# Kernel tuning notes

Measured on AMD Instinct MI355X. Metric: run time of the kernel, lower is better.

Reference implementation:

```python
import jax, jax.numpy as jnp
import numpy as np

N_HEAD = 8
D_MODEL = 128  # per-head dim == d_model in this 'interpretable' MHA
B, S = 2, 2048
LN_EPS = 1e-3  # keras LayerNormalization default epsilon


def setup_inputs() -> dict:
    key = jax.random.key(0)
    ks = jax.random.split(key, 8)
    sc = 1.0 / np.sqrt(D_MODEL)
    q = jax.random.normal(ks[0], (B, S, D_MODEL), jnp.float32)
    k = jax.random.normal(ks[1], (B, S, D_MODEL), jnp.float32)
    v = jax.random.normal(ks[2], (B, S, D_MODEL), jnp.float32)
    # multiplicative causal mask (lower-triangular ones), broadcast over B,H
    mask = jnp.tril(jnp.ones((S, S), jnp.float32))[None, None, :, :]
    Wq = jax.random.normal(ks[3], (D_MODEL, N_HEAD * D_MODEL), jnp.float32) * sc
    Wk = jax.random.normal(ks[4], (D_MODEL, N_HEAD * D_MODEL), jnp.float32) * sc
    Wv = jax.random.normal(ks[5], (D_MODEL, N_HEAD * D_MODEL), jnp.float32) * sc
    Wo = jax.random.normal(ks[6], (N_HEAD * D_MODEL, D_MODEL), jnp.float32) * sc
    gamma = jnp.ones((D_MODEL,), jnp.float32)
    beta = jnp.zeros((D_MODEL,), jnp.float32)
    return {"q": q, "k": k, "v": v, "mask": mask, "Wq": Wq, "Wk": Wk,
            "Wv": Wv, "Wo": Wo, "gamma": gamma, "beta": beta}


def reference(q, k, v, mask, Wq, Wk, Wv, Wo, gamma, beta):
    b = q.shape[0]
    # projections -> [B, H, S, D]
    def split_heads(x):
        return x.reshape(b, -1, N_HEAD, D_MODEL).transpose(0, 2, 1, 3)
    qs = split_heads(q @ Wq)
    ks_ = split_heads(k @ Wk)
    vs = split_heads(v @ Wv)
    scores = jnp.einsum('bhqd,bhkd->bhqk', qs, ks_) / jnp.sqrt(jnp.float32(D_MODEL))
    scores = scores * mask  # multiplicative mask (NOT additive -inf)
    attn = jax.nn.softmax(scores, axis=-1)
    # dropout layers are identity at inference
    out = jnp.einsum('bhqk,bhkd->bhqd', attn, vs)
    out = out.transpose(0, 2, 1, 3).reshape(b, -1, N_HEAD * D_MODEL)
    out = out @ Wo
    # keras LayerNorm (axis=-1, eps=1e-3)
    mu = jnp.mean(out, axis=-1, keepdims=True)
    var = jnp.var(out, axis=-1, keepdims=True)
    out = (out - mu) * jax.lax.rsqrt(var + LN_EPS) * gamma + beta
    return out
```

## Files before the change

### kernel.cpp

```cpp
#include <hip/hip_runtime.h>
#include <math.h>

#define B 2
#define S 2048
#define H 8
#define D 128
#define DM 1024
#define BH 16

typedef unsigned short u16;
typedef __attribute__((ext_vector_type(8))) short bf16x8;
typedef __attribute__((ext_vector_type(8))) unsigned short u16x8;
typedef __attribute__((ext_vector_type(4))) float f32x4;

__device__ __forceinline__ float bf2f(u16 x) {
    union { unsigned u; float f; } c; c.u = ((unsigned)x) << 16; return c.f;
}
__device__ __forceinline__ u16 f2bf(float f) {
    union { unsigned u; float f; } c; c.f = f;
    unsigned u = c.u; u += 0x7fffu + ((u >> 16) & 1u);
    return (u16)(u >> 16);
}
__device__ __forceinline__ u16 ftr(float f) {
    union { unsigned u; float f; } c; c.f = f;
    return (u16)(c.u >> 16);
}

#define MFMA16(a, b, c) __builtin_amdgcn_mfma_f32_16x16x32_bf16((a), (b), (c), 0, 0, 0)

__global__ __launch_bounds__(256) void prep_kernel(
    const float* __restrict__ Wq, const float* __restrict__ Wk, const float* __restrict__ Wv,
    const float* __restrict__ Wo, u16* __restrict__ WT, u16* __restrict__ WoT)
{
    __shared__ __align__(16) u16 Wl[128][132];
    int tid = threadIdx.x, by = blockIdx.x;
    if (by < 16) {
        int k0 = by * 64;
#pragma unroll
        for (int i = 0; i < 8; i++) {
            int e = i * 256 + tid; int kk = e >> 5, n4 = e & 31;
            float4 w4 = *(const float4*)&Wo[(size_t)(k0 + kk) * D + n4 * 4];
            ushort4 p; p.x = ftr(w4.x); p.y = ftr(w4.y); p.z = ftr(w4.z); p.w = ftr(w4.w);
            *(ushort4*)&Wl[kk][n4 * 4] = p;
        }
        __syncthreads();
#pragma unroll
        for (int i = 0; i < 4; i++) {
            int e = i * 256 + tid; int n = e >> 3, ko = e & 7;
            u16x8 g;
#pragma unroll
            for (int j = 0; j < 8; j++) g[j] = Wl[ko * 8 + j][n];
            *(u16x8*)&WoT[(size_t)n * DM + k0 + ko * 8] = g;
        }
    } else {
        int tile = by - 16;
        int t = tile >> 3, h = tile & 7;
        const float* W = (t == 0) ? Wq : (t == 1) ? Wk : Wv;
        int col0 = h * 128;
#pragma unroll
        for (int i = 0; i < 16; i++) {
            int e = i * 256 + tid; int kk = e >> 5, n4 = e & 31;
            float4 w4 = *(const float4*)&W[(size_t)kk * DM + col0 + n4 * 4];
            ushort4 p; p.x = ftr(w4.x); p.y = ftr(w4.y); p.z = ftr(w4.z); p.w = ftr(w4.w);
            *(ushort4*)&Wl[kk][n4 * 4] = p;
        }
        __syncthreads();
        u16* WTt = WT + (size_t)tile * (128 * 128);
#pragma unroll
        for (int i = 0; i < 8; i++) {
            int e = i * 256 + tid; int n = e >> 4, ko = e & 15;
            u16x8 g;
#pragma unroll
            for (int j = 0; j < 8; j++) g[j] = Wl[ko * 8 + j][n];
            *(u16x8*)&WTt[(size_t)n * 128 + ko * 8] = g;
        }
    }
}

__global__ __launch_bounds__(256) void proj_kernel(
    const float* __restrict__ q, const float* __restrict__ k, const float* __restrict__ v,
    const u16* __restrict__ WT,
    u16* __restrict__ Qo, u16* __restrict__ Ko, u16* __restrict__ VTo,
    float* __restrict__ Csum)
{
    __shared__ __align__(16) u16 Xs[128][136];
    __shared__ __align__(16) u16 Ws[128][136];
    int tid = threadIdx.x;
    int m0 = blockIdx.x * 128;
    int by = blockIdx.y;
    int t = by >> 3;
    int h = by & 7;
    const float* X = (t == 0) ? q : (t == 1) ? k : v;
    const u16* WTt = WT + (size_t)(t * 8 + h) * (128 * 128);

#pragma unroll
    for (int i = 0; i < 16; i++) {
        int e = i * 256 + tid; int r = e >> 5, c4 = e & 31;
        float4 x4 = *(const float4*)&X[(size_t)(m0 + r) * D + c4 * 4];
        ushort4 p; p.x = ftr(x4.x); p.y = ftr(x4.y); p.z = ftr(x4.z); p.w = ftr(x4.w);
        *(ushort4*)&Xs[r][c4 * 4] = p;
    }
#pragma unroll
    for (int i = 0; i < 8; i++) {
        int e = i * 256 + tid; int n = e >> 4, c8 = e & 15;
        *(u16x8*)&Ws[n][c8 * 8] = *(const u16x8*)&WTt[(size_t)n * 128 + c8 * 8];
    }
    __syncthreads();

    int w = tid >> 6, lane = tid & 63, quad = lane >> 4, ln = lane & 15;
    bf16x8 aX[2][4];
#pragma unroll
    for (int rf = 0; rf < 2; rf++)
#pragma unroll
        for (int ks = 0; ks < 4; ks++)
            aX[rf][ks] = *(const bf16x8*)&Xs[w * 32 + rf * 16 + ln][ks * 32 + quad * 8];

    f32x4 zero = {0.f, 0.f, 0.f, 0.f};
    f32x4 acc[2][8];
#pragma unroll
    for (int rf = 0; rf < 2; rf++)
#pragma unroll
        for (int nt = 0; nt < 8; nt++) acc[rf][nt] = zero;

#pragma unroll
    for (int ks = 0; ks < 4; ks++) {
        bf16x8 bW[8];
#pragma unroll
        for (int nt = 0; nt < 8; nt++)
            bW[nt] = *(const bf16x8*)&Ws[nt * 16 + ln][ks * 32 + quad * 8];
#pragma unroll
        for (int nt = 0; nt < 8; nt++) {
            acc[0][nt] = MFMA16(aX[0][ks], bW[nt], acc[0][nt]);
            acc[1][nt] = MFMA16(aX[1][ks], bW[nt], acc[1][nt]);
        }
    }

    int bb = m0 >> 11, ss0 = m0 & 2047;
    int bh = bb * 8 + h;
    __syncthreads();
    u16 (*Ct)[136] = Xs;
    if (t < 2) {
        u16* O = (t == 0) ? Qo : Ko;
#pragma unroll
        for (int rf = 0; rf < 2; rf++)
#pragma unroll
            for (int nt = 0; nt < 8; nt++)
#pragma unroll
                for (int r = 0; r < 4; r++)
                    Ct[w * 32 + rf * 16 + quad * 4 + r][nt * 16 + ln] = f2bf(acc[rf][nt][r]);
        __syncthreads();
#pragma unroll
        for (int i = 0; i < 8; i++) {
            int e = i * 256 + tid; int r = e >> 4, c8 = e & 15;
            *(u16x8*)&O[((size_t)bh * S + ss0 + r) * D + c8 * 8] = *(const u16x8*)&Ct[r][c8 * 8];
        }
    } else {
#pragma unroll
        for (int rf = 0; rf < 2; rf++)
#pragma unroll
            for (int nt = 0; nt < 8; nt++)
#pragma unroll
                for (int r = 0; r < 4; r++)
                    Ct[nt * 16 + ln][w * 32 + rf * 16 + quad * 4 + r] = f2bf(acc[rf][nt][r]);
        __syncthreads();
#pragma unroll
        for (int i = 0; i < 8; i++) {
            int e = i * 256 + tid; int dloc = e >> 4, s8 = e & 15;
            *(u16x8*)&VTo[((size_t)bh * D + dloc) * S + ss0 + s8 * 8] =
                *(const u16x8*)&Ct[dloc][s8 * 8];
        }
        {
            int d = tid >> 1, c = tid & 1;
            float s = 0.f;
#pragma unroll
            for (int i = 0; i < 8; i++) {
                u16x8 v8 = *(const u16x8*)&Ct[d][c * 64 + i * 8];
#pragma unroll
                for (int j = 0; j < 8; j++) s += bf2f(v8[j]);
            }
            Csum[((size_t)bh * 32 + (ss0 >> 6) + c) * D + d] = s;
        }
    }
}

__global__ __launch_bounds__(256, 3) void attn_kernel(
    const u16* __restrict__ Qb, const u16* __restrict__ Kb, const u16* __restrict__ VTg,
    const float* __restrict__ Csum, u16* __restrict__ HOb)
{
    __shared__ __align__(16) u16 Ks[64][136];
    __shared__ __align__(16) u16 Vt[128][72];
    __shared__ __align__(16) u16 Ps[4][16][72];

    int tid = threadIdx.x;
    int qb = 31 - blockIdx.x;
    int bh = blockIdx.y;
    int q0 = qb * 64;
    int nt = (qb & ~1) + 2;
    int w = tid >> 6, lane = tid & 63, quad = lane >> 4, ln = lane & 15;
    const u16* Qp  = Qb  + (size_t)bh * S * D;
    const u16* Kp  = Kb  + (size_t)bh * S * D;
    const u16* VTp = VTg + (size_t)bh * D * S;

    bf16x8 aQ[4];
    int qrow = q0 + w * 16 + ln;
#pragma unroll
    for (int ks = 0; ks < 4; ks++)
        aQ[ks] = *(const bf16x8*)&Qp[(size_t)qrow * D + ks * 32 + quad * 8];

    f32x4 zero = {0.f, 0.f, 0.f, 0.f};
    f32x4 accPV[8], acc_l[4];
#pragma unroll
    for (int jd = 0; jd < 8; jd++) accPV[jd] = zero;
#pragma unroll
    for (int g = 0; g < 4; g++) acc_l[g] = zero;
    bf16x8 bOnes;
#pragma unroll
    for (int j = 0; j < 8; j++) bOnes[j] = (short)0x3F80;
    const float scale = 0.08838834764831845f;

    for (int kt = 0; kt < nt; kt++) {
        __syncthreads();
        int k0 = kt * 64;
#pragma unroll
        for (int i = 0; i < 4; i++) {
            int e = i * 256 + tid; int r = e >> 4, c8 = e & 15;
            *(u16x8*)&Ks[r][c8 * 8] = *(const u16x8*)&Kp[(size_t)(k0 + r) * D + c8 * 8];
        }
#pragma unroll
        for (int i = 0; i < 4; i++) {
            int e = i * 256 + tid; int dd = e >> 3, c8 = e & 7;
            *(u16x8*)&Vt[dd][c8 * 8] = *(const u16x8*)&VTp[(size_t)dd * S + k0 + c8 * 8];
        }
        __syncthreads();

#pragma unroll
        for (int ct = 0; ct < 4; ct++) {
            f32x4 s = zero;
#pragma unroll
            for (int ks = 0; ks < 4; ks++) {
                bf16x8 bK = *(const bf16x8*)&Ks[ct * 16 + ln][ks * 32 + quad * 8];
                s = MFMA16(aQ[ks], bK, s);
            }
            int col = k0 + ct * 16 + ln;
            int rowb = q0 + w * 16 + quad * 4;
#pragma unroll
            for (int r = 0; r < 4; r++) {
                float tv = (col <= rowb + r) ? s[r] : 0.f;
                Ps[w][quad * 4 + r][ct * 16 + ln] = f2bf(__expf(tv * scale));
            }
        }
#pragma unroll
        for (int ks = 0; ks < 2; ks++) {
            bf16x8 aP = *(const bf16x8*)&Ps[w][ln][ks * 32 + quad * 8];
            int g = (2 * kt + ks) & 3;
            acc_l[g] = MFMA16(aP, bOnes, acc_l[g]);
#pragma unroll
            for (int jd = 0; jd < 8; jd++) {
                bf16x8 vf = *(const bf16x8*)&Vt[jd * 16 + ln][ks * 32 + quad * 8];
                accPV[jd] = MFMA16(aP, vf, accPV[jd]);
            }
        }
    }

    float suf[8];
#pragma unroll
    for (int jd = 0; jd < 8; jd++) suf[jd] = 0.f;
    for (int c = 31; c >= nt; c--) {
        const float* cp = &Csum[((size_t)(bh * 32 + c)) * D + ln];
#pragma unroll
        for (int jd = 0; jd < 8; jd++) suf[jd] += cp[jd * 16];
    }
    int scount = S - nt * 64;
    int b = bh >> 3, h = bh & 7;
#pragma unroll
    for (int r = 0; r < 4; r++) {
        int srow = q0 + w * 16 + quad * 4 + r;
        float l = ((acc_l[0][r] + acc_l[1][r]) + acc_l[2][r]) + acc_l[3][r] + (float)scount;
        float inv = 1.f / l;
        size_t base = ((size_t)(b * S + srow)) * DM + h * D;
#pragma unroll
        for (int jd = 0; jd < 8; jd++)
            HOb[base + jd * 16 + ln] = f2bf((accPV[jd][r] + suf[jd]) * inv);
    }
}

__global__ __launch_bounds__(256) void out_ln_kernel(
    const u16* __restrict__ HOb, const u16* __restrict__ WoT,
    const float* __restrict__ gamma, const float* __restrict__ beta,
    float* __restrict__ out)
{
    __shared__ __align__(16) u16 HOs[16][1048];
    __shared__ float Cs[16][132];
    int tid = threadIdx.x;
    int m0 = blockIdx.x * 16;
    int w = tid >> 6, lane = tid & 63, quad = lane >> 4, ln = lane & 15;
#pragma unroll
    for (int i = 0; i < 8; i++) {
        int e = i * 256 + tid; int r = e >> 7, c8 = e & 127;
        *(u16x8*)&HOs[r][c8 * 8] = *(const u16x8*)&HOb[(size_t)(m0 + r) * DM + c8 * 8];
    }
    __syncthreads();
    f32x4 zero = {0.f, 0.f, 0.f, 0.f};
    f32x4 acc[2] = {zero, zero};
#pragma unroll 4
    for (int ks = 0; ks < 32; ks++) {
        bf16x8 aH = *(const bf16x8*)&HOs[ln][ks * 32 + quad * 8];
        bf16x8 w0 = *(const bf16x8*)&WoT[(size_t)(w * 32 + ln) * DM + ks * 32 + quad * 8];
        bf16x8 w1 = *(const bf16x8*)&WoT[(size_t)(w * 32 + 16 + ln) * DM + ks * 32 + quad * 8];
        acc[0] = MFMA16(aH, w0, acc[0]);
        acc[1] = MFMA16(aH, w1, acc[1]);
    }
#pragma unroll
    for (int ct = 0; ct < 2; ct++)
#pragma unroll
        for (int r = 0; r < 4; r++)
            Cs[quad * 4 + r][w * 32 + ct * 16 + ln] = acc[ct][r];
    __syncthreads();

    int row = tid >> 4, t16 = tid & 15;
    float xv[8], sum = 0.f, sq = 0.f;
#pragma unroll
    for (int j = 0; j < 8; j++) {
        float x = Cs[row][t16 * 8 + j];
        xv[j] = x; sum += x; sq += x * x;
    }
#pragma unroll
    for (int off = 1; off < 16; off <<= 1) {
        sum += __shfl_xor(sum, off);
        sq  += __shfl_xor(sq, off);
    }
    float mu = sum * (1.f / 128.f);
    float var = sq * (1.f / 128.f) - mu * mu;
    float rstd = rsqrtf(var + 1e-3f);
    float o[8];
#pragma unroll
    for (int j = 0; j < 8; j++) {
        int c = t16 * 8 + j;
        o[j] = (xv[j] - mu) * rstd * gamma[c] + beta[c];
    }
    float* op = &out[(size_t)(m0 + row) * D + t16 * 8];
    *(float4*)&op[0] = *(float4*)&o[0];
    *(float4*)&op[4] = *(float4*)&o[4];
}

extern "C" void kernel_launch(void* const* d_in, const int* in_sizes, int n_in,
                              void* d_out, int out_size, void* d_ws, size_t ws_size,
                              hipStream_t stream)
{
    const float* q     = (const float*)d_in[0];
    const float* k     = (const float*)d_in[1];
    const float* v     = (const float*)d_in[2];
    const float* Wq    = (const float*)d_in[4];
    const float* Wk    = (const float*)d_in[5];
    const float* Wv    = (const float*)d_in[6];
    const float* Wo    = (const float*)d_in[7];
    const float* gamma = (const float*)d_in[8];
    const float* beta  = (const float*)d_in[9];

    u16* ws16 = (u16*)d_ws;
    u16* Qb  = ws16;
    u16* Kb  = ws16 + 4194304;
    u16* VT  = ws16 + 8388608;
    u16* HOb = ws16 + 12582912;
    u16* WoT = ws16 + 16777216;
    u16* WT  = ws16 + 16908288;
    float* Csum = (float*)((char*)d_ws + 35651584);

    prep_kernel<<<40, 256, 0, stream>>>(Wq, Wk, Wv, Wo, WT, WoT);
    proj_kernel<<<dim3(32, 24), 256, 0, stream>>>(q, k, v, WT, Qb, Kb, VT, Csum);
    attn_kernel<<<dim3(32, BH), 256, 0, stream>>>(Qb, Kb, VT, Csum, HOb);
    out_ln_kernel<<<256, 256, 0, stream>>>(HOb, WoT, gamma, beta, (float*)d_out);
}
```

Before: 178.4 us.

## Pair causal query tiles per block, widen K/V tiles, prefetch via registers

Each 512-thread block now handles two query tiles, one high and one low, so every block does a balanced amount of causal work and shares the K/V tiles loaded into LDS between both. Key tiles grow from 64 to 128 rows, and the next tile's K/V are prefetched into registers while the current one is computed, which overlaps global loads with the MFMA work. The grid is reordered with the head index fastest. In exchange, LDS and register use per block rise, occupancy is lower, and the warps of the low tile sit idle while they wait at barriers after their last tile.

New measurement: 158.4 us. -11.2%, faster.

```diff
diff --git a/kernel.cpp b/kernel.cpp
--- a/kernel.cpp
+++ b/kernel.cpp
@@ -183,26 +183,30 @@
     }
 }
 
-__global__ __launch_bounds__(256, 3) void attn_kernel(
+__global__ __launch_bounds__(512, 2) void attn_kernel(
     const u16* __restrict__ Qb, const u16* __restrict__ Kb, const u16* __restrict__ VTg,
     const float* __restrict__ Csum, u16* __restrict__ HOb)
 {
-    __shared__ __align__(16) u16 Ks[64][136];
-    __shared__ __align__(16) u16 Vt[128][72];
-    __shared__ __align__(16) u16 Ps[4][16][72];
+    __shared__ __align__(16) u16 Ks[128][136];
+    __shared__ __align__(16) u16 Vt[128][136];
+    __shared__ __align__(16) u16 Ps[8][16][40];
 
     int tid = threadIdx.x;
-    int qb = 31 - blockIdx.x;
-    int bh = blockIdx.y;
+    int bh = blockIdx.x;
+    int bx = blockIdx.y;
+    int w = tid >> 6, lane = tid & 63, quad = lane >> 4, ln = lane & 15;
+    int qt = w >> 2, wq = w & 3;
+    int qb = qt ? bx : (31 - bx);
     int q0 = qb * 64;
-    int nt = (qb & ~1) + 2;
-    int w = tid >> 6, lane = tid & 63, quad = lane >> 4, ln = lane & 15;
+    int nhi = ((31 - bx) >> 1) + 1;
+    int nlo = (bx >> 1) + 1;
+    int nq = qt ? nlo : nhi;
     const u16* Qp  = Qb  + (size_t)bh * S * D;
     const u16* Kp  = Kb  + (size_t)bh * S * D;
     const u16* VTp = VTg + (size_t)bh * D * S;
 
     bf16x8 aQ[4];
-    int qrow = q0 + w * 16 + ln;
+    int qrow = q0 + wq * 16 + ln;
 #pragma unroll
     for (int ks = 0; ks < 4; ks++)
         aQ[ks] = *(const bf16x8*)&Qp[(size_t)qrow * D + ks * 32 + quad * 8];
@@ -218,63 +222,79 @@
     for (int j = 0; j < 8; j++) bOnes[j] = (short)0x3F80;
     const float scale = 0.08838834764831845f;
 
-    for (int kt = 0; kt < nt; kt++) {
-        __syncthreads();
-        int k0 = kt * 64;
+    int e0 = w * 256 + lane;
+    u16x8 regK[4], regV[4];
+#pragma unroll
+    for (int i = 0; i < 4; i++) {
+        int e = e0 + i * 64;
+        regK[i] = *(const u16x8*)&Kp[(size_t)e * 8];
+        regV[i] = *(const u16x8*)&VTp[(size_t)(e >> 4) * S + (e & 15) * 8];
+    }
+
+    for (int kt = 0; kt < nhi; kt++) {
+        __syncthreads();
 #pragma unroll
         for (int i = 0; i < 4; i++) {
-            int e = i * 256 + tid; int r = e >> 4, c8 = e & 15;
-            *(u16x8*)&Ks[r][c8 * 8] = *(const u16x8*)&Kp[(size_t)(k0 + r) * D + c8 * 8];
-        }
-#pragma unroll
-        for (int i = 0; i < 4; i++) {
-            int e = i * 256 + tid; int dd = e >> 3, c8 = e & 7;
-            *(u16x8*)&Vt[dd][c8 * 8] = *(const u16x8*)&VTp[(size_t)dd * S + k0 + c8 * 8];
-        }
-        __syncthreads();
-
-#pragma unroll
-        for (int ct = 0; ct < 4; ct++) {
-            f32x4 s = zero;
-#pragma unroll
-            for (int ks = 0; ks < 4; ks++) {
-                bf16x8 bK = *(const bf16x8*)&Ks[ct * 16 + ln][ks * 32 + quad * 8];
-                s = MFMA16(aQ[ks], bK, s);
+            int e = e0 + i * 64;
+            *(u16x8*)&Ks[e >> 4][(e & 15) * 8] = regK[i];
+            *(u16x8*)&Vt[e >> 4][(e & 15) * 8] = regV[i];
+        }
+        if (kt + 1 < nhi) {
+            int k0n = (kt + 1) * 128;
+#pragma unroll
+            for (int i = 0; i < 4; i++) {
+                int e = e0 + i * 64;
+                regK[i] = *(const u16x8*)&Kp[(size_t)k0n * D + (size_t)e * 8];
+                regV[i] = *(const u16x8*)&VTp[(size_t)(e >> 4) * S + k0n + (e & 15) * 8];
             }
-            int col = k0 + ct * 16 + ln;
-            int rowb = q0 + w * 16 + quad * 4;
-#pragma unroll
-            for (int r = 0; r < 4; r++) {
-                float tv = (col <= rowb + r) ? s[r] : 0.f;
-                Ps[w][quad * 4 + r][ct * 16 + ln] = f2bf(__expf(tv * scale));
+        }
+        __syncthreads();
+
+        if (qt == 0 || kt < nlo) {
+            int k0 = kt * 128;
+            int rowb = q0 + wq * 16 + quad * 4;
+#pragma unroll
+            for (int ks2 = 0; ks2 < 4; ks2++) {
+#pragma unroll
+                for (int ct2 = 0; ct2 < 2; ct2++) {
+                    f32x4 s = zero;
+#pragma unroll
+                    for (int ks = 0; ks < 4; ks++) {
+                        bf16x8 bK = *(const bf16x8*)&Ks[ks2 * 32 + ct2 * 16 + ln][ks * 32 + quad * 8];
+                        s = MFMA16(aQ[ks], bK, s);
+                    }
+                    int col = k0 + ks2 * 32 + ct2 * 16 + ln;
+#pragma unroll
+                    for (int r = 0; r < 4; r++) {
+                        float tv = (col <= rowb + r) ? s[r] : 0.f;
+                        Ps[w][quad * 4 + r][ct2 * 16 + ln] = f2bf(__expf(tv * scale));
+                    }
+                }
+                bf16x8 aP = *(const bf16x8*)&Ps[w][ln][quad * 8];
+                acc_l[ks2] = MFMA16(aP, bOnes, acc_l[ks2]);
+#pragma unroll
+                for (int jd = 0; jd < 8; jd++) {
+                    bf16x8 vf = *(const bf16x8*)&Vt[jd * 16 + ln][ks2 * 32 + quad * 8];
+                    accPV[jd] = MFMA16(aP, vf, accPV[jd]);
+                }
             }
         }
-#pragma unroll
-        for (int ks = 0; ks < 2; ks++) {
-            bf16x8 aP = *(const bf16x8*)&Ps[w][ln][ks * 32 + quad * 8];
-            int g = (2 * kt + ks) & 3;
-            acc_l[g] = MFMA16(aP, bOnes, acc_l[g]);
-#pragma unroll
-            for (int jd = 0; jd < 8; jd++) {
-                bf16x8 vf = *(const bf16x8*)&Vt[jd * 16 + ln][ks * 32 + quad * 8];
-                accPV[jd] = MFMA16(aP, vf, accPV[jd]);
-            }
-        }
-    }
-
+    }
+
+    int nt64 = 2 * nq;
     float suf[8];
 #pragma unroll
     for (int jd = 0; jd < 8; jd++) suf[jd] = 0.f;
-    for (int c = 31; c >= nt; c--) {
+    for (int c = 31; c >= nt64; c--) {
         const float* cp = &Csum[((size_t)(bh * 32 + c)) * D + ln];
 #pragma unroll
         for (int jd = 0; jd < 8; jd++) suf[jd] += cp[jd * 16];
     }
-    int scount = S - nt * 64;
+    int scount = S - nq * 128;
     int b = bh >> 3, h = bh & 7;
 #pragma unroll
     for (int r = 0; r < 4; r++) {
-        int srow = q0 + w * 16 + quad * 4 + r;
+        int srow = q0 + wq * 16 + quad * 4 + r;
         float l = ((acc_l[0][r] + acc_l[1][r]) + acc_l[2][r]) + acc_l[3][r] + (float)scount;
         float inv = 1.f / l;
         size_t base = ((size_t)(b * S + srow)) * DM + h * D;
@@ -368,6 +388,6 @@
 
     prep_kernel<<<40, 256, 0, stream>>>(Wq, Wk, Wv, Wo, WT, WoT);
     proj_kernel<<<dim3(32, 24), 256, 0, stream>>>(q, k, v, WT, Qb, Kb, VT, Csum);
-    attn_kernel<<<dim3(32, BH), 256, 0, stream>>>(Qb, Kb, VT, Csum, HOb);
+    attn_kernel<<<dim3(BH, 16), 512, 0, stream>>>(Qb, Kb, VT, Csum, HOb);
     out_ln_kernel<<<256, 256, 0, stream>>>(HOb, WoT, gamma, beta, (float*)d_out);
 }
```
